# Optimization experiments

Measured on AMD Instinct MI355X. Metric: run time of the kernel, lower is better.

Reference implementation:

```python
import jax, jax.numpy as jnp
import numpy as np


def _made_masks(D, H):
    # Standard MADE masks, natural ordering, param_count=2 (shift, log_scale).
    d_in = np.arange(1, D + 1)                      # input degrees 1..D
    d_h = (np.arange(H) % (D - 1)) + 1              # hidden degrees cycle 1..D-1
    d_out = np.tile(d_in, 2)                        # output degrees, 2 params per dim
    M1 = (d_h[None, :] >= d_in[:, None]).astype(np.float32)   # [D, H]
    M2 = (d_out[None, :] > d_h[:, None]).astype(np.float32)
    return jnp.asarray(M1), jnp.asarray(M2)


def setup_inputs() -> dict:
    key = jax.random.key(0)
    B, D, H = 4096, 1024, 4096
    k0, k1, k2 = jax.random.split(key, 3)
    z = jax.random.normal(k0, (B, D), dtype=jnp.float32)
    W1 = jax.random.normal(k1, (D, H), dtype=jnp.float32) * (1.0 / np.sqrt(D))
    b1 = jnp.zeros((H,), dtype=jnp.float32)
    # small init on output layer keeps exp(log_scale) well-conditioned
    W2 = jax.random.normal(k2, (H, 2 * D), dtype=jnp.float32) * (0.1 / np.sqrt(H))
    b2 = jnp.zeros((2 * D,), dtype=jnp.float32)
    permutation = jnp.arange(D, dtype=jnp.int32)
    return {"z": z, "W1": W1, "b1": b1, "W2": W2, "b2": b2, "permutation": permutation}


def reference(z, W1, b1, W2, b2, permutation):
    # IAR.forward_flow: permute -> MADE masked MLP -> split params -> affine transform -> inverse permute
    D = z.shape[1]
    H = W1.shape[1]
    M1, M2 = _made_masks(D, H)
    zp = z[:, permutation]                          # permute_data
    h = jax.nn.relu(zp @ (W1 * M1) + b1)            # [B, H]
    res = h @ (W2 * M2) + b2                        # [B, 2D]
    mu, log_s = res[:, :D], res[:, D:]              # res.split(dim_in, dim=1)
    x = zp * jnp.exp(log_s) + mu                    # affine transform, forward=True
    log_det = jnp.sum(log_s, axis=1)                # [B]
    inv = jnp.argsort(permutation)                  # inv_permute_data
    return x[:, inv], log_det
```

## Files before the change

### kernel.cpp

```cpp
#include <hip/hip_runtime.h>
#include <stdint.h>


typedef float   f32x4  __attribute__((ext_vector_type(4)));
typedef int     i32x4  __attribute__((ext_vector_type(4)));
typedef int     i32x8  __attribute__((ext_vector_type(8)));

__device__ __forceinline__ uint8_t f2fp8(float f) {
    int p = __builtin_amdgcn_cvt_pk_fp8_f32(f, 0.0f, 0, false);
    return (uint8_t)(p & 0xff);
}
__device__ __forceinline__ int8_t f2i8(float v, float s) {
    float q = rintf(v * s);
    q = fminf(fmaxf(q, -127.0f), 127.0f);
    return (int8_t)q;
}

#define GLD16(g, l)                                                          \
    __builtin_amdgcn_global_load_lds(                                        \
        (const __attribute__((address_space(1))) uint32_t*)(g),              \
        (__attribute__((address_space(3))) uint32_t*)(l), 16, 0, 0)

#define MFMA_MX(a, b, c)                                                     \
    __builtin_amdgcn_mfma_scale_f32_16x16x128_f8f6f4(                        \
        (a), (b), (c), 0, 0, 0, 0x7F7F7F7F, 0, 0x7F7F7F7F)

__global__ __launch_bounds__(256) void prep_k(
    const float* __restrict__ W1, int8_t* __restrict__ W1mT,
    const float* __restrict__ W2, uint8_t* __restrict__ W2mT,
    float* __restrict__ ws2p,
    const float* __restrict__ z, const int* __restrict__ perm,
    int8_t* __restrict__ zp, float* __restrict__ ld,
    int D, int H, int B) {
    const int bx  = blockIdx.x;
    const int tid = threadIdx.x;
    const int NB1 = (H / 64) * (D / 64);
    const int NB2 = (2 * D / 64) * (H / 64);

    if (bx < NB1) {
        __shared__ int8_t t[64][68];
        const int c0 = (bx % (H / 64)) * 64;
        const int r0 = (bx / (H / 64)) * 64;
        const int q  = tid & 15;
        const int r  = tid >> 4;

        const int fid = bx * 256 + tid;
        if (fid < B) ld[fid] = 0.0f;

#pragma unroll
        for (int rr0 = 0; rr0 < 64; rr0 += 16) {
            const int rr  = rr0 + r;
            const int row = r0 + rr;
            const float4 v4 =
                *(const float4*)&W1[(size_t)row * H + c0 + q * 4];
            const float vv[4] = {v4.x, v4.y, v4.z, v4.w};
            union { int8_t b4[4]; uint32_t u; } pk;
#pragma unroll
            for (int j = 0; j < 4; j++) {
                const int c = c0 + q * 4 + j;
                pk.b4[j] = ((c % (D - 1)) >= row) ? f2i8(vv[j], 1024.0f)
                                                  : (int8_t)0;
            }
            *(uint32_t*)&t[rr][q * 4] = pk.u;
        }
        __syncthreads();
#pragma unroll
        for (int pass = 0; pass < 2; pass++) {
            const int cc = pass * 32 + (tid >> 3);
            const int j0 = (tid & 7) * 8;
            union { int8_t b[8]; uint64_t qq; } v;
#pragma unroll
            for (int j = 0; j < 8; j++) v.b[j] = t[j0 + j][cc];
            *(uint64_t*)&W1mT[(size_t)(c0 + cc) * D + r0 + j0] = v.qq;
        }
    } else if (bx < NB1 + NB2) {
        __shared__ uint8_t t[64][68];
        const int idx = bx - NB1;
        const int c0 = (idx % (2 * D / 64)) * 64;
        const int r0 = (idx / (2 * D / 64)) * 64;
        const int q  = tid & 15;
        const int r  = tid >> 4;
        const bool second = (c0 >= D);
        const int cb = (c0 - D) >> 6;

#pragma unroll
        for (int rr0 = 0; rr0 < 64; rr0 += 16) {
            const int rr  = rr0 + r;
            const int row = r0 + rr;
            const float4 v4 =
                *(const float4*)&W2[(size_t)row * 2 * D + c0 + q * 4];
            const float vv[4] = {v4.x, v4.y, v4.z, v4.w};
            union { uint8_t b4[4]; uint32_t u; } pk;
            float s = 0.0f;
#pragma unroll
            for (int j = 0; j < 4; j++) {
                const int c = c0 + q * 4 + j;
                const bool keep = ((c % D) > (row % (D - 1)));
                pk.b4[j] = keep ? f2fp8(vv[j] * 256.0f) : (uint8_t)0;
                s += keep ? vv[j] : 0.0f;
            }
            *(uint32_t*)&t[rr][q * 4] = pk.u;
            if (second) {
#pragma unroll
                for (int o = 8; o > 0; o >>= 1) s += __shfl_down(s, o, 16);
                if (q == 0) ws2p[(size_t)cb * H + row] = s;
            }
        }
        __syncthreads();
#pragma unroll
        for (int pass = 0; pass < 2; pass++) {
            const int cc = pass * 32 + (tid >> 3);
            const int j0 = (tid & 7) * 8;
            union { uint8_t b[8]; uint64_t qq; } v;
#pragma unroll
            for (int j = 0; j < 8; j++) v.b[j] = t[j0 + j][cc];
            *(uint64_t*)&W2mT[(size_t)(c0 + cc) * H + r0 + j0] = v.qq;
        }
    } else {
        const int bp = bx - NB1 - NB2;
        const int i0 = tid * 4;
        const int4 p4 = *(const int4*)(perm + i0);
#pragma unroll
        for (int rr = 0; rr < 2; rr++) {
            const int b = bp * 2 + rr;
            const float* zr = z + (size_t)b * D;
            union { int8_t b4[4]; uint32_t u; } q;
            q.b4[0] = f2i8(zr[p4.x], 32.0f);
            q.b4[1] = f2i8(zr[p4.y], 32.0f);
            q.b4[2] = f2i8(zr[p4.z], 32.0f);
            q.b4[3] = f2i8(zr[p4.w], 32.0f);
            *(uint32_t*)&zp[(size_t)b * D + i0] = q.u;
        }
    }
}

__global__ __launch_bounds__(256) void gemm1_k(
    const int8_t* __restrict__ A, const int8_t* __restrict__ Bt,
    const float* __restrict__ bias, const float* __restrict__ ws2p,
    uint8_t* __restrict__ Cout, float* __restrict__ ld,
    int M, int N, int K) {
    __shared__ __align__(16) int8_t Alds[128 * 128];
    __shared__ __align__(16) int8_t Blds[128 * 128];
    __shared__ float pdl[128];

    const int id   = blockIdx.x;
    const int xcd  = id & 7, s = id >> 3;
    const int mb   = s & 31;
    const int nb   = xcd * 4 + (s >> 5);
    const int m0   = mb * 128;
    const int n0   = nb * 128;

    const int tid  = threadIdx.x;
    const int lane = tid & 63;
    const int w    = tid >> 6;
    const int wm   = (w & 1) * 64;
    const int wn   = (w >> 1) * 64;
    const int quad = lane >> 4;
    const int l16  = lane & 15;

    i32x4 acc[4][4];
#pragma unroll
    for (int i = 0; i < 4; i++)
#pragma unroll
        for (int j = 0; j < 4; j++) acc[i][j] = (i32x4)0;

    const int8_t* Ag[4];
    const int8_t* Bg[4];
    int8_t *Al[4], *Bl[4];
#pragma unroll
    for (int k = 0; k < 4; k++) {
        const int c  = tid + k * 256;
        const int so = ((c & 7) ^ ((c >> 3) & 7)) * 16;
        Ag[k] = A + (size_t)(m0 + (c >> 3)) * K + so;
        Bg[k] = Bt + (size_t)(n0 + (c >> 3)) * K + so;
        Al[k] = &Alds[c * 16];
        Bl[k] = &Blds[c * 16];
    }

    const int sw   = l16 & 7;
    const int arow = (wm + l16) * 128;
    const int brow = (wn + l16) * 128;

    for (int kt = 0; kt < K; kt += 128) {
        __syncthreads();
#pragma unroll
        for (int k = 0; k < 4; k++) {
            GLD16(Ag[k] + kt, Al[k]);
            GLD16(Bg[k] + kt, Bl[k]);
        }
        __syncthreads();

#pragma unroll
        for (int kh = 0; kh < 2; kh++) {
            const int pc = ((kh * 4 + quad) ^ sw) * 16;
            i32x4 af[4], bfr[4];
#pragma unroll
            for (int mi = 0; mi < 4; mi++)
                af[mi] = *(const i32x4*)&Alds[arow + mi * 16 * 128 + pc];
#pragma unroll
            for (int ni = 0; ni < 4; ni++)
                bfr[ni] = *(const i32x4*)&Blds[brow + ni * 16 * 128 + pc];
#pragma unroll
            for (int mi = 0; mi < 4; mi++)
#pragma unroll
                for (int ni = 0; ni < 4; ni++)
                    acc[mi][ni] = __builtin_amdgcn_mfma_i32_16x16x64_i8(
                        af[mi], bfr[ni], acc[mi][ni], 0, 0, 0);
        }
    }

    const float inv = 1.0f / 32768.0f;
    float bv[4], wv[4];
#pragma unroll
    for (int ni = 0; ni < 4; ni++) {
        const int col = n0 + wn + ni * 16 + l16;
        bv[ni] = bias[col];
        float sv = 0.0f;
#pragma unroll
        for (int cb = 0; cb < 16; cb++) sv += ws2p[(size_t)cb * N + col];
        wv[ni] = sv;
    }
    float pd[4][4];
#pragma unroll
    for (int mi = 0; mi < 4; mi++)
#pragma unroll
        for (int r = 0; r < 4; r++) pd[mi][r] = 0.0f;

#pragma unroll
    for (int mi = 0; mi < 4; mi++) {
        const int row = m0 + wm + mi * 16 + quad * 4;
#pragma unroll
        for (int ni = 0; ni < 4; ni++) {
            const int col = n0 + wn + ni * 16 + l16;
#pragma unroll
            for (int r = 0; r < 4; r++) {
                float v = fmaxf((float)acc[mi][ni][r] * inv + bv[ni], 0.0f);
                pd[mi][r] += v * wv[ni];
                Cout[(size_t)(row + r) * N + col] = f2fp8(v);
            }
        }
    }

#pragma unroll
    for (int off = 1; off < 16; off <<= 1)
#pragma unroll
        for (int mi = 0; mi < 4; mi++)
#pragma unroll
            for (int r = 0; r < 4; r++)
                pd[mi][r] += __shfl_xor(pd[mi][r], off, 16);

    __syncthreads();
    if ((w >> 1) == 0 && l16 == 0)
#pragma unroll
        for (int mi = 0; mi < 4; mi++)
#pragma unroll
            for (int r = 0; r < 4; r++)
                pdl[wm + mi * 16 + quad * 4 + r] = pd[mi][r];
    __syncthreads();
    if ((w >> 1) == 1 && l16 == 0)
#pragma unroll
        for (int mi = 0; mi < 4; mi++)
#pragma unroll
            for (int r = 0; r < 4; r++)
                pdl[wm + mi * 16 + quad * 4 + r] += pd[mi][r];
    __syncthreads();
    if (tid < 128) atomicAdd(&ld[m0 + tid], pdl[tid]);
}

__global__ __launch_bounds__(256) void gemm2f_k(
    const uint8_t* __restrict__ A, const uint8_t* __restrict__ Bt,
    const float* __restrict__ b2, const int* __restrict__ perm,
    const float* __restrict__ z, const float* __restrict__ ld,
    float* __restrict__ out, int B, int D, int K) {
    __shared__ __align__(16) uint8_t Alds[2][128 * 128];
    __shared__ __align__(16) uint8_t Blds[2][128 * 128];
    __shared__ float red[4];

    const int id   = blockIdx.x;
    const int nb   = id & 15;
    const int s    = id >> 4;
    const int m0   = s * 128;
    const int p0   = nb * 64;

    const int tid  = threadIdx.x;
    const int lane = tid & 63;
    const int w    = tid >> 6;
    const int wm   = (w & 1) * 64;
    const int wp   = (w >> 1) * 32;
    const int quad = lane >> 4;
    const int l16  = lane & 15;

    f32x4 acc[4][4];
#pragma unroll
    for (int i = 0; i < 4; i++)
#pragma unroll
        for (int j = 0; j < 4; j++) acc[i][j] = (f32x4)0.0f;

    const uint8_t* Ag[4];
    const uint8_t* Bg[4];
    int ldso[4];
#pragma unroll
    for (int k = 0; k < 4; k++) {
        const int c  = tid + k * 256;
        const int r  = c >> 3;
        const int so = ((c & 7) ^ (r & 7)) * 16;
        Ag[k] = A + (size_t)(m0 + r) * K + so;
        const int g = (r < 64) ? (p0 + r) : (D + p0 + (r - 64));
        Bg[k] = Bt + (size_t)g * K + so;
        ldso[k] = c * 16;
    }

    const int sw   = l16 & 7;
    const int pc0  = ((quad * 2) ^ sw) * 16;
    const int pc1  = ((quad * 2 + 1) ^ sw) * 16;

#pragma unroll
    for (int k = 0; k < 4; k++) {
        GLD16(Ag[k], &Alds[0][ldso[k]]);
        GLD16(Bg[k], &Blds[0][ldso[k]]);
    }
#pragma unroll
    for (int k = 0; k < 4; k++) {
        GLD16(Ag[k] + 128, &Alds[1][ldso[k]]);
        GLD16(Bg[k] + 128, &Blds[1][ldso[k]]);
    }

    const int NT = K / 128;
    for (int t = 0; t < NT; ++t) {
        if (t < NT - 1) {
            asm volatile("s_waitcnt vmcnt(8)" ::: "memory");
        } else {
            asm volatile("s_waitcnt vmcnt(0)" ::: "memory");
        }
        asm volatile("s_barrier" ::: "memory");

        const int cur = t & 1;
        union ABu { int4 h2[2]; i32x8 v; };
        i32x8 af[4], bfr[4];
#pragma unroll
        for (int mi = 0; mi < 4; mi++) {
            ABu tt;
            const int ar = (wm + mi * 16 + l16) * 128;
            tt.h2[0] = *(const int4*)&Alds[cur][ar + pc0];
            tt.h2[1] = *(const int4*)&Alds[cur][ar + pc1];
            af[mi] = tt.v;
        }
#pragma unroll
        for (int ni = 0; ni < 4; ni++) {
            ABu tt;
            const int br = ((ni >> 1) * 64 + wp + (ni & 1) * 16 + l16) * 128;
            tt.h2[0] = *(const int4*)&Blds[cur][br + pc0];
            tt.h2[1] = *(const int4*)&Blds[cur][br + pc1];
            bfr[ni] = tt.v;
        }
        __builtin_amdgcn_s_setprio(1);
#pragma unroll
        for (int mi = 0; mi < 4; mi++)
#pragma unroll
            for (int ni = 0; ni < 4; ni++)
                acc[mi][ni] = MFMA_MX(af[mi], bfr[ni], acc[mi][ni]);
        __builtin_amdgcn_s_setprio(0);

        if (t + 2 < NT) {
            asm volatile("s_barrier" ::: "memory");
#pragma unroll
            for (int k = 0; k < 4; k++) {
                GLD16(Ag[k] + (t + 2) * 128, &Alds[cur][ldso[k]]);
                GLD16(Bg[k] + (t + 2) * 128, &Blds[cur][ldso[k]]);
            }
        }
    }

    const float inv = 1.0f / 256.0f;
    float bmu[2], bls[2];
    int   pcv[2];
#pragma unroll
    for (int ci = 0; ci < 2; ci++) {
        const int gc = p0 + wp + ci * 16 + l16;
        bmu[ci] = b2[gc];
        bls[ci] = b2[D + gc];
        pcv[ci] = perm[gc];
    }
#pragma unroll
    for (int mi = 0; mi < 4; mi++) {
        const int row0 = m0 + wm + mi * 16 + quad * 4;
#pragma unroll
        for (int ci = 0; ci < 2; ci++) {
#pragma unroll
            for (int r = 0; r < 4; r++) {
                const size_t idx = (size_t)(row0 + r) * D + pcv[ci];
                const float mu = acc[mi][ci][r] * inv + bmu[ci];
                float ls = acc[mi][ci + 2][r] * inv + bls[ci];
                ls = fminf(fmaxf(ls, -30.0f), 30.0f);
                out[idx] = z[idx] * expf(ls) + mu;
            }
        }
    }

    if (nb == 0) {
        float bs = 0.0f;
        for (int i = tid; i < D; i += 256) bs += b2[D + i];
#pragma unroll
        for (int o = 32; o > 0; o >>= 1) bs += __shfl_down(bs, o, 64);
        if ((tid & 63) == 0) red[tid >> 6] = bs;
        __syncthreads();
        if (tid < 128)
            out[(size_t)B * D + m0 + tid] =
                ld[m0 + tid] + red[0] + red[1] + red[2] + red[3];
    }
}

extern "C" void kernel_launch(void* const* d_in, const int* in_sizes, int n_in,
                              void* d_out, int out_size, void* d_ws, size_t ws_size,
                              hipStream_t stream) {
    const float* z    = (const float*)d_in[0];
    const float* W1   = (const float*)d_in[1];
    const float* b1   = (const float*)d_in[2];
    const float* W2   = (const float*)d_in[3];
    const float* b2   = (const float*)d_in[4];
    const int*   perm = (const int*)d_in[5];
    float* out = (float*)d_out;
    char*  ws  = (char*)d_ws;

    const int D = in_sizes[5];
    const int H = in_sizes[2];
    const int B = in_sizes[0] / D;

    const size_t off_h    = 0;
    const size_t off_W2mT = off_h    + (size_t)B * H;
    const size_t off_W1mT = off_W2mT + (size_t)2 * D * H;
    const size_t off_zp   = off_W1mT + (size_t)H * D;
    const size_t off_ws2  = off_zp   + (size_t)B * D;
    const size_t off_ld   = off_ws2  + (size_t)16 * H * 4;

    uint8_t* h    = (uint8_t*)(ws + off_h);
    uint8_t* W2mT = (uint8_t*)(ws + off_W2mT);
    int8_t*  W1mT = (int8_t*)(ws + off_W1mT);
    int8_t*  zp   = (int8_t*)(ws + off_zp);
    float*   ws2p = (float*)(ws + off_ws2);
    float*   ld   = (float*)(ws + off_ld);

    const int NB1 = (H / 64) * (D / 64);
    const int NB2 = (2 * D / 64) * (H / 64);
    const int NBP = B / 2;
    prep_k<<<NB1 + NB2 + NBP, 256, 0, stream>>>(
        W1, W1mT, W2, W2mT, ws2p, z, perm, zp, ld, D, H, B);

    gemm1_k<<<(H / 128) * (B / 128), 256, 0, stream>>>(
        zp, W1mT, b1, ws2p, h, ld, B, H, D);

    gemm2f_k<<<(D / 64) * (B / 128), 256, 0, stream>>>(
        h, W2mT, b2, perm, z, ld, out, B, D, H);
}
```

Before: 172.1 us.

## Double-buffer LDS tiles in int8 GEMM1 with prefetch two stages ahead

Converts the GEMM1 main loop from load-then-compute with two barriers per K tile into a two-stage LDS ring. The next tile's global_load_lds transfers stay in flight while MFMAs run, using a partial vmcnt wait and raw s_barrier. The MFMA block is also wrapped in s_setprio to favour issue. This doubles LDS use to about 64KB per block, which may reduce occupancy. The manual waitcnt/barrier ordering depends on exactly eight outstanding loads per thread.

```diff
diff --git a/kernel.cpp b/kernel.cpp
--- a/kernel.cpp
+++ b/kernel.cpp
@@ -139,8 +139,8 @@
     const float* __restrict__ bias, const float* __restrict__ ws2p,
     uint8_t* __restrict__ Cout, float* __restrict__ ld,
     int M, int N, int K) {
-    __shared__ __align__(16) int8_t Alds[128 * 128];
-    __shared__ __align__(16) int8_t Blds[128 * 128];
+    __shared__ __align__(16) int8_t Alds[2][128 * 128];
+    __shared__ __align__(16) int8_t Blds[2][128 * 128];
     __shared__ float pdl[128];
 
     const int id   = blockIdx.x;
@@ -166,46 +166,68 @@
 
     const int8_t* Ag[4];
     const int8_t* Bg[4];
-    int8_t *Al[4], *Bl[4];
+    int ldso[4];
 #pragma unroll
     for (int k = 0; k < 4; k++) {
         const int c  = tid + k * 256;
         const int so = ((c & 7) ^ ((c >> 3) & 7)) * 16;
         Ag[k] = A + (size_t)(m0 + (c >> 3)) * K + so;
         Bg[k] = Bt + (size_t)(n0 + (c >> 3)) * K + so;
-        Al[k] = &Alds[c * 16];
-        Bl[k] = &Blds[c * 16];
+        ldso[k] = c * 16;
     }
 
     const int sw   = l16 & 7;
     const int arow = (wm + l16) * 128;
     const int brow = (wn + l16) * 128;
 
-    for (int kt = 0; kt < K; kt += 128) {
-        __syncthreads();
-#pragma unroll
-        for (int k = 0; k < 4; k++) {
-            GLD16(Ag[k] + kt, Al[k]);
-            GLD16(Bg[k] + kt, Bl[k]);
-        }
-        __syncthreads();
-
+#pragma unroll
+    for (int k = 0; k < 4; k++) {
+        GLD16(Ag[k], &Alds[0][ldso[k]]);
+        GLD16(Bg[k], &Blds[0][ldso[k]]);
+    }
+#pragma unroll
+    for (int k = 0; k < 4; k++) {
+        GLD16(Ag[k] + 128, &Alds[1][ldso[k]]);
+        GLD16(Bg[k] + 128, &Blds[1][ldso[k]]);
+    }
+
+    const int NT = K / 128;
+    for (int t = 0; t < NT; ++t) {
+        if (t < NT - 1) {
+            asm volatile("s_waitcnt vmcnt(8)" ::: "memory");
+        } else {
+            asm volatile("s_waitcnt vmcnt(0)" ::: "memory");
+        }
+        asm volatile("s_barrier" ::: "memory");
+
+        const int cur = t & 1;
 #pragma unroll
         for (int kh = 0; kh < 2; kh++) {
             const int pc = ((kh * 4 + quad) ^ sw) * 16;
             i32x4 af[4], bfr[4];
 #pragma unroll
             for (int mi = 0; mi < 4; mi++)
-                af[mi] = *(const i32x4*)&Alds[arow + mi * 16 * 128 + pc];
+                af[mi] = *(const i32x4*)&Alds[cur][arow + mi * 16 * 128 + pc];
 #pragma unroll
             for (int ni = 0; ni < 4; ni++)
-                bfr[ni] = *(const i32x4*)&Blds[brow + ni * 16 * 128 + pc];
+                bfr[ni] = *(const i32x4*)&Blds[cur][brow + ni * 16 * 128 + pc];
+            __builtin_amdgcn_s_setprio(1);
 #pragma unroll
             for (int mi = 0; mi < 4; mi++)
 #pragma unroll
                 for (int ni = 0; ni < 4; ni++)
                     acc[mi][ni] = __builtin_amdgcn_mfma_i32_16x16x64_i8(
                         af[mi], bfr[ni], acc[mi][ni], 0, 0, 0);
+            __builtin_amdgcn_s_setprio(0);
+        }
+
+        if (t + 2 < NT) {
+            asm volatile("s_barrier" ::: "memory");
+#pragma unroll
+            for (int k = 0; k < 4; k++) {
+                GLD16(Ag[k] + (t + 2) * 128, &Alds[cur][ldso[k]]);
+                GLD16(Bg[k] + (t + 2) * 128, &Blds[cur][ldso[k]]);
+            }
         }
     }
 
```

Measured after the change: 169.4 us, median of 2. Within noise of the previous version (-1.6%).
